# Optimization experiments

Measured on AMD Instinct MI355X. Metric: run time of the kernel, lower is better.

The kernel has to match this reference:

```python
import jax, jax.numpy as jnp
import numpy as np

B, S, D = 2, 2048, 1024   # batch, seq, hidden_dim
I = 512                   # intermediate_dim (per-expert FFN width)
E = 16                    # num_experts
TOP_K = 2


def setup_inputs() -> dict:
    key = jax.random.key(0)
    ks = jax.random.split(key, 10)
    sc_d = 1.0 / np.sqrt(D)
    sc_i = 1.0 / np.sqrt(I)
    return {
        "x": jax.random.normal(ks[0], (B, S, D), dtype=jnp.float32),
        # router gate: Linear(D -> E) with bias (nnx.Linear default)
        "gate_w": jax.random.normal(ks[1], (D, E), dtype=jnp.float32) * sc_d,
        "gate_b": jnp.zeros((E,), dtype=jnp.float32),
        # shared expert MLP (SwiGLU: down(silu(gate(x)) * up(x)))
        "shared_wg": jax.random.normal(ks[2], (D, I), dtype=jnp.float32) * sc_d,
        "shared_wu": jax.random.normal(ks[3], (D, I), dtype=jnp.float32) * sc_d,
        "shared_wd": jax.random.normal(ks[4], (I, D), dtype=jnp.float32) * sc_i,
        # routed experts, stacked on leading E axis
        "experts_wg": jax.random.normal(ks[5], (E, D, I), dtype=jnp.float32) * sc_d,
        "experts_wu": jax.random.normal(ks[6], (E, D, I), dtype=jnp.float32) * sc_d,
        "experts_wd": jax.random.normal(ks[7], (E, I, D), dtype=jnp.float32) * sc_i,
    }


def _mlp(x, wg, wu, wd):
    # SwiGLU MLP: down(silu(gate(x)) * up(x))
    return jnp.einsum("bsi,id->bsd", jax.nn.silu(x @ wg) * (x @ wu), wd)


def reference(x, gate_w, gate_b, shared_wg, shared_wu, shared_wd,
              experts_wg, experts_wu, experts_wd):
    # router: sigmoid logits -> top_k -> normalize by sum of selected scores
    router_logits = jax.nn.sigmoid(x @ gate_w + gate_b)          # [B,S,E]
    expert_values, expert_indices = jax.lax.top_k(router_logits, k=TOP_K)
    expert_values = expert_values / jnp.sum(expert_values, axis=-1, keepdims=True)

    # dense all-expert compute (faithful to source): [B,S,E,D]
    hg = jnp.einsum("bsd,edi->bsei", x, experts_wg)
    hu = jnp.einsum("bsd,edi->bsei", x, experts_wu)
    all_outputs = jnp.einsum("bsei,eid->bsed", jax.nn.silu(hg) * hu, experts_wd)

    # gather top-k expert outputs: [B,S,K,D]
    selected = jnp.take_along_axis(all_outputs, expert_indices[..., None], axis=2)
    expert_weighted = jnp.sum(expert_values[..., None] * selected, axis=2)  # [B,S,D]

    return x + _mlp(x, shared_wg, shared_wu, shared_wd) + expert_weighted
```

## Files before the change

kernel.cpp:

```cpp
#include <hip/hip_runtime.h>
#include <stdint.h>

typedef __attribute__((ext_vector_type(8))) short short8;
typedef __attribute__((ext_vector_type(4))) float f32x4;

#define TOKENS 4096
#define DDIM 1024
#define IDIM 512
#define NEXP 16
#define NEXP1 17
#define CSTRIDE 32
#define MAXMB 112

#define OFF_WGU   0ull
#define OFF_WD    35651584ull
#define OFF_XB    53477376ull
#define OFF_HGU   61865984ull
#define OFF_H     87031808ull
#define OFF_TOK   99614720ull
#define OFF_REC   99893248ull
#define OFF_WREC  99926016ull
#define OFF_CNT   100171776ull
#define OFF_BASE  100175872ull

__device__ __forceinline__ float bf2f(unsigned short u) {
    union { uint32_t i; float f; } v; v.i = ((uint32_t)u) << 16; return v.f;
}
__device__ __forceinline__ unsigned short f2bf(float f) {
    union { float f; uint32_t i; } v; v.f = f;
    uint32_t r = v.i + 0x7FFFu + ((v.i >> 16) & 1u);
    return (unsigned short)(r >> 16);
}
__device__ __forceinline__ void cp16(const unsigned short* g, unsigned short* l) {
    __builtin_amdgcn_global_load_lds(
        (const __attribute__((address_space(1))) uint32_t*)g,
        (__attribute__((address_space(3))) uint32_t*)l, 16, 0, 0);
}

__global__ __launch_bounds__(256)
void k_transpose(const float* __restrict__ eg, const float* __restrict__ eu,
                 const float* __restrict__ ed, const float* __restrict__ sg,
                 const float* __restrict__ su, const float* __restrict__ sd,
                 unsigned short* __restrict__ Wgu, unsigned short* __restrict__ Wd)
{
    int z = blockIdx.z;
    int e = z / 3, m = z % 3;
    int R = (m == 2) ? 512 : 1024;
    int C = (m == 2) ? 1024 : 512;
    int r0 = blockIdx.y * 64, c0 = blockIdx.x * 64;
    if (r0 >= R || c0 >= C) return;
    const float* src;
    if (m == 0)      src = (e < 16) ? eg + (size_t)e * 524288 : sg;
    else if (m == 1) src = (e < 16) ? eu + (size_t)e * 524288 : su;
    else             src = (e < 16) ? ed + (size_t)e * 524288 : sd;

    __shared__ float tl[64 * 65];
    const int tid = threadIdx.x;

    {
        const int lr = tid >> 4;
        const int lc = (tid & 15) * 4;
        #pragma unroll
        for (int ps = 0; ps < 4; ++ps) {
            int r = ps * 16 + lr;
            float4 v = *(const float4*)(src + (size_t)(r0 + r) * C + (c0 + lc));
            float* d = &tl[r * 65 + lc];
            d[0] = v.x; d[1] = v.y; d[2] = v.z; d[3] = v.w;
        }
    }
    __syncthreads();

    {
        const int w = tid >> 6, l = tid & 63;
        const int kb = (l & 7) * 8;
        #pragma unroll
        for (int p = 0; p < 2; ++p) {
            int nl = p * 32 + w * 8 + (l >> 3);
            unsigned short ov[8];
            #pragma unroll
            for (int j = 0; j < 8; ++j)
                ov[j] = f2bf(tl[(kb + j) * 65 + nl]);
            int n = c0 + nl;
            int k = r0 + kb;
            unsigned short* dst;
            if (m < 2) dst = Wgu + (size_t)e * 1048576 + (size_t)(2 * n + m) * 1024 + k;
            else       dst = Wd  + (size_t)e * 524288  + (size_t)n * 512 + k;
            *(uint4*)dst = *(uint4*)ov;
        }
    }
}

__global__ void k_xconv(const float* __restrict__ x, unsigned short* __restrict__ xb,
                        int* __restrict__ tok)
{
    int i = blockIdx.x * 256 + threadIdx.x;
    float4 v = ((const float4*)x)[i];
    ushort4 b;
    b.x = f2bf(v.x); b.y = f2bf(v.y); b.z = f2bf(v.z); b.w = f2bf(v.w);
    ((ushort4*)xb)[i] = b;
    if (i < TOKENS) tok[16 * 4096 + i] = i;
}

__global__ __launch_bounds__(512, 4)
void k_router(const float* __restrict__ x, const float* __restrict__ gw,
              const float* __restrict__ gb, int* __restrict__ tok,
              int2* __restrict__ rec, float2* __restrict__ wrec,
              int* __restrict__ counts)
{
    __shared__ float gws[1024 * 12];

    const int t = blockIdx.x * 8 + (threadIdx.x >> 6);
    const int lane = threadIdx.x & 63;
    const float* xr = x + (size_t)t * DDIM;

    float xv[16];
    #pragma unroll
    for (int kk = 0; kk < 16; ++kk) xv[kk] = xr[kk * 64 + lane];

    float v[16];

    for (int p = 0; p < 2; ++p) {
        __syncthreads();
        #pragma unroll
        for (int c = 0; c < 4; ++c) {
            int idx = threadIdx.x + c * 512;
            int k = idx >> 1;
            int h = (idx & 1) * 4;
            float4 g4 = *(const float4*)(gw + k * 16 + p * 8 + h);
            *(float4*)&gws[k * 12 + h] = g4;
        }
        __syncthreads();

        double a[8];
        #pragma unroll
        for (int j = 0; j < 8; ++j) a[j] = 0.0;

        #pragma unroll
        for (int kk = 0; kk < 16; ++kk) {
            int kl = kk * 64 + lane;
            float4 gA = *(const float4*)&gws[kl * 12];
            float4 gB = *(const float4*)&gws[kl * 12 + 4];
            double xd = (double)xv[kk];
            a[0] += xd * (double)gA.x; a[1] += xd * (double)gA.y;
            a[2] += xd * (double)gA.z; a[3] += xd * (double)gA.w;
            a[4] += xd * (double)gB.x; a[5] += xd * (double)gB.y;
            a[6] += xd * (double)gB.z; a[7] += xd * (double)gB.w;
        }

        #pragma unroll
        for (int off = 32; off > 0; off >>= 1) {
            #pragma unroll
            for (int j = 0; j < 8; ++j)
                a[j] += __shfl_xor(a[j], off, 64);
        }

        #pragma unroll
        for (int j = 0; j < 8; ++j)
            v[p * 8 + j] = 1.0f / (1.0f + expf(-(float)(a[j] + (double)gb[p * 8 + j])));
    }

    if (lane == 0) {
        int i0 = 0;
        #pragma unroll
        for (int e = 1; e < 16; ++e) if (v[e] > v[i0]) i0 = e;
        int i1 = (i0 == 0) ? 1 : 0;
        #pragma unroll
        for (int e = 0; e < 16; ++e) if (e != i0 && e != i1 && v[e] > v[i1]) i1 = e;
        float s = v[i0] + v[i1];
        float w0 = v[i0] / s, w1 = v[i1] / s;
        int p0 = atomicAdd(&counts[i0 * CSTRIDE], 1);
        tok[i0 * 4096 + p0] = t;
        int p1 = atomicAdd(&counts[i1 * CSTRIDE], 1);
        tok[i1 * 4096 + p1] = t;
        rec[t]  = make_int2(i0 * 4096 + p0, i1 * 4096 + p1);
        wrec[t] = make_float2(w0, w1);
    }
}

__global__ void k_prefix(int* counts, int* bases, int* mbp)
{
    if (threadIdx.x == 0 && blockIdx.x == 0) {
        counts[16 * CSTRIDE] = TOKENS;
        int a = 0, b = 0;
        for (int e = 0; e < NEXP1; ++e) {
            int c = counts[e * CSTRIDE];
            bases[e] = a; a += c;
            mbp[e] = b;  b += (c + 127) >> 7;
        }
        bases[17] = a;
        mbp[17] = b;
    }
}

template <int MODE>
__global__ __launch_bounds__(256, 3)
void k_gemm(const unsigned short* __restrict__ Amat, const unsigned short* __restrict__ Bmat,
            const int* __restrict__ tok, const int* __restrict__ counts,
            const int* __restrict__ bases, const int* __restrict__ mbp,
            unsigned short* __restrict__ Out)
{
    constexpr int K = (MODE == 0) ? 1024 : 512;
    const int my = blockIdx.y;
    if (my >= mbp[17]) return;
    int e = 0;
    while (my >= mbp[e + 1]) ++e;
    const int cnt = counts[e * CSTRIDE];
    const int m0 = (my - mbp[e]) * 128;
    const int n0 = blockIdx.x * 128;
    const int base = bases[e];

    __shared__ unsigned short As0[128 * 32];
    __shared__ unsigned short As1[128 * 32];
    __shared__ unsigned short Bs0[128 * 32];
    __shared__ unsigned short Bs1[128 * 32];

    const int tid  = threadIdx.x;
    const int wave = tid >> 6;
    const int lane = tid & 63;
    const int lrow = lane >> 2;
    const int lseg = lane & 3;

    unsigned short* a0d0 = &As0[wave * 1024];
    unsigned short* a0d1 = &As0[wave * 1024 + 512];
    unsigned short* a1d0 = &As1[wave * 1024];
    unsigned short* a1d1 = &As1[wave * 1024 + 512];
    unsigned short* b0d0 = &Bs0[wave * 1024];
    unsigned short* b0d1 = &Bs0[wave * 1024 + 512];
    unsigned short* b1d0 = &Bs1[wave * 1024];
    unsigned short* b1d1 = &Bs1[wave * 1024 + 512];

    int ar0 = m0 + wave * 32 + lrow;      if (ar0 > cnt - 1) ar0 = cnt - 1;
    int ar1 = m0 + wave * 32 + 16 + lrow; if (ar1 > cnt - 1) ar1 = cnt - 1;
    size_t ai0, ai1;
    if (MODE == 0) { ai0 = (size_t)tok[e * 4096 + ar0]; ai1 = (size_t)tok[e * 4096 + ar1]; }
    else           { ai0 = (size_t)(base + ar0);        ai1 = (size_t)(base + ar1); }
    const unsigned short* ag0 = Amat + ai0 * K + lseg * 8;
    const unsigned short* ag1 = Amat + ai1 * K + lseg * 8;
    const size_t eoff = (size_t)e * 1024 * K;
    const unsigned short* bg0 = Bmat + eoff + (size_t)(n0 + wave * 32 + lrow) * K + lseg * 8;
    const unsigned short* bg1 = Bmat + eoff + (size_t)(n0 + wave * 32 + 16 + lrow) * K + lseg * 8;

    const int wm = wave & 1, wn = wave >> 1;
    const int q = lane >> 4, mc = lane & 15;

    f32x4 acc[4][4];
    #pragma unroll
    for (int i = 0; i < 4; ++i)
        #pragma unroll
        for (int j = 0; j < 4; ++j) acc[i][j] = (f32x4){0.f, 0.f, 0.f, 0.f};

    for (int k0 = 0; k0 < K; k0 += 64) {
        __syncthreads();
        cp16(ag0 + k0,      a0d0);
        cp16(ag0 + k0 + 32, a1d0);
        cp16(ag1 + k0,      a0d1);
        cp16(ag1 + k0 + 32, a1d1);
        cp16(bg0 + k0,      b0d0);
        cp16(bg0 + k0 + 32, b1d0);
        cp16(bg1 + k0,      b0d1);
        cp16(bg1 + k0 + 32, b1d1);
        __syncthreads();
        short8 a0[4], b0[4], a1[4], b1[4];
        #pragma unroll
        for (int i = 0; i < 4; ++i) {
            a0[i] = *(const short8*)&As0[(wm * 64 + i * 16 + mc) * 32 + q * 8];
            a1[i] = *(const short8*)&As1[(wm * 64 + i * 16 + mc) * 32 + q * 8];
        }
        #pragma unroll
        for (int j = 0; j < 4; ++j) {
            b0[j] = *(const short8*)&Bs0[(wn * 64 + j * 16 + mc) * 32 + q * 8];
            b1[j] = *(const short8*)&Bs1[(wn * 64 + j * 16 + mc) * 32 + q * 8];
        }
        #pragma unroll
        for (int i = 0; i < 4; ++i)
            #pragma unroll
            for (int j = 0; j < 4; ++j)
                acc[i][j] = __builtin_amdgcn_mfma_f32_16x16x32_bf16(a0[i], b0[j], acc[i][j], 0, 0, 0);
        #pragma unroll
        for (int i = 0; i < 4; ++i)
            #pragma unroll
            for (int j = 0; j < 4; ++j)
                acc[i][j] = __builtin_amdgcn_mfma_f32_16x16x32_bf16(a1[i], b1[j], acc[i][j], 0, 0, 0);
    }

    #pragma unroll
    for (int i = 0; i < 4; ++i) {
        int lr = wm * 64 + i * 16 + q * 4;
        #pragma unroll
        for (int r = 0; r < 4; ++r) {
            int mrow = m0 + lr + r;
            if (mrow >= cnt) continue;
            #pragma unroll
            for (int j = 0; j < 4; ++j) {
                int gc = n0 + wn * 64 + j * 16 + mc;
                float val = acc[i][j][r];
                if (MODE == 0) {
                    float other = __shfl_xor(val, 1, 64);
                    float g = (mc & 1) ? other : val;
                    float u = (mc & 1) ? val : other;
                    float h = g / (1.0f + __expf(-g)) * u;
                    if ((mc & 1) == 0)
                        Out[(size_t)(base + mrow) * 512 + (gc >> 1)] = f2bf(h);
                } else {
                    Out[(size_t)(base + mrow) * 1024 + gc] = f2bf(val);
                }
            }
        }
    }
}

__global__ void k_combine(const float* __restrict__ x, const unsigned short* __restrict__ Hs,
                          const int2* __restrict__ rec, const float2* __restrict__ wrec,
                          const int* __restrict__ bases, float* __restrict__ out)
{
    int t = blockIdx.x * 2 + (threadIdx.x >> 7);
    int c = (threadIdx.x & 127) * 8;
    int2 r = rec[t];
    float2 w = wrec[t];
    int s0 = bases[r.x >> 12] + (r.x & 4095);
    int s1 = bases[r.y >> 12] + (r.y & 4095);
    int ss = 8192 + t;

    unsigned short h0[8], h1[8], hs[8];
    *(uint4*)h0 = *(const uint4*)(Hs + (size_t)s0 * 1024 + c);
    *(uint4*)h1 = *(const uint4*)(Hs + (size_t)s1 * 1024 + c);
    *(uint4*)hs = *(const uint4*)(Hs + (size_t)ss * 1024 + c);
    const float* xr = x + (size_t)t * 1024 + c;
    float o[8];
    #pragma unroll
    for (int j = 0; j < 8; ++j)
        o[j] = xr[j] + bf2f(hs[j]) + w.x * bf2f(h0[j]) + w.y * bf2f(h1[j]);
    float* orow = out + (size_t)t * 1024 + c;
    *(float4*)orow       = *(float4*)&o[0];
    *(float4*)(orow + 4) = *(float4*)&o[4];
}

extern "C" void kernel_launch(void* const* d_in, const int* in_sizes, int n_in,
                              void* d_out, int out_size, void* d_ws, size_t ws_size,
                              hipStream_t stream)
{
    const float* x  = (const float*)d_in[0];
    const float* gw = (const float*)d_in[1];
    const float* gb = (const float*)d_in[2];
    const float* sg = (const float*)d_in[3];
    const float* su = (const float*)d_in[4];
    const float* sd = (const float*)d_in[5];
    const float* eg = (const float*)d_in[6];
    const float* eu = (const float*)d_in[7];
    const float* ed = (const float*)d_in[8];
    float* out = (float*)d_out;
    char* ws = (char*)d_ws;

    unsigned short* Wgu = (unsigned short*)(ws + OFF_WGU);
    unsigned short* Wd  = (unsigned short*)(ws + OFF_WD);
    unsigned short* xb  = (unsigned short*)(ws + OFF_XB);
    unsigned short* Hgu = (unsigned short*)(ws + OFF_HGU);
    unsigned short* H   = (unsigned short*)(ws + OFF_H);
    int*    tok   = (int*)(ws + OFF_TOK);
    int2*   rec   = (int2*)(ws + OFF_REC);
    float2* wrec  = (float2*)(ws + OFF_WREC);
    int*    counts= (int*)(ws + OFF_CNT);
    int*    bases = (int*)(ws + OFF_BASE);
    int*    mbp   = bases + 20;

    hipMemsetAsync(counts, 0, 4096, stream);
    k_transpose<<<dim3(16, 16, 51), 256, 0, stream>>>(eg, eu, ed, sg, su, sd, Wgu, Wd);
    k_xconv<<<4096, 256, 0, stream>>>(x, xb, tok);
    k_router<<<512, 512, 0, stream>>>(x, gw, gb, tok, rec, wrec, counts);
    k_prefix<<<1, 64, 0, stream>>>(counts, bases, mbp);
    k_gemm<0><<<dim3(8, MAXMB), 256, 0, stream>>>(xb, Wgu, tok, counts, bases, mbp, H);
    k_gemm<1><<<dim3(8, MAXMB), 256, 0, stream>>>(H, Wd, tok, counts, bases, mbp, Hgu);
    k_combine<<<2048, 256, 0, stream>>>(x, Hgu, rec, wrec, bases, out);
}
```

Measured before the change: 282.6 us.

## Double-buffer LDS tiles with prefetch and XOR-swizzle shared memory layout

```diff
diff --git a/kernel.cpp b/kernel.cpp
--- a/kernel.cpp
+++ b/kernel.cpp
@@ -192,8 +192,45 @@
     }
 }
 
+
+#define STAGE8(BUF, KK) do {                                                  \
+    cp16(ag0 + (KK),      &As[BUF][0][wb]);                                   \
+    cp16(ag0 + (KK) + 32, &As[BUF][1][wb]);                                   \
+    cp16(ag1 + (KK),      &As[BUF][0][wb + 512]);                             \
+    cp16(ag1 + (KK) + 32, &As[BUF][1][wb + 512]);                             \
+    cp16(bg0 + (KK),      &Bs[BUF][0][wb]);                                   \
+    cp16(bg0 + (KK) + 32, &Bs[BUF][1][wb]);                                   \
+    cp16(bg1 + (KK),      &Bs[BUF][0][wb + 512]);                             \
+    cp16(bg1 + (KK) + 32, &Bs[BUF][1][wb + 512]);                             \
+} while (0)
+
+#define GSTEP(BUF, PRE, KNEXT) do {                                           \
+    if (PRE) STAGE8((BUF) ^ 1, KNEXT);                                        \
+    short8 va0[4], va1[4], vb0[4], vb1[4];                                    \
+    _Pragma("unroll")                                                         \
+    for (int i = 0; i < 4; ++i) {                                             \
+        va0[i] = *(const short8*)&As[BUF][0][(wm*64 + i*16 + mc)*32 + qs];    \
+        va1[i] = *(const short8*)&As[BUF][1][(wm*64 + i*16 + mc)*32 + qs];    \
+    }                                                                         \
+    _Pragma("unroll")                                                         \
+    for (int j = 0; j < 4; ++j) {                                             \
+        vb0[j] = *(const short8*)&Bs[BUF][0][(wn*64 + j*16 + mc)*32 + qs];    \
+        vb1[j] = *(const short8*)&Bs[BUF][1][(wn*64 + j*16 + mc)*32 + qs];    \
+    }                                                                         \
+    _Pragma("unroll")                                                         \
+    for (int i = 0; i < 4; ++i)                                               \
+        _Pragma("unroll")                                                     \
+        for (int j = 0; j < 4; ++j)                                           \
+            acc[i][j] = __builtin_amdgcn_mfma_f32_16x16x32_bf16(va0[i], vb0[j], acc[i][j], 0, 0, 0); \
+    _Pragma("unroll")                                                         \
+    for (int i = 0; i < 4; ++i)                                               \
+        _Pragma("unroll")                                                     \
+        for (int j = 0; j < 4; ++j)                                           \
+            acc[i][j] = __builtin_amdgcn_mfma_f32_16x16x32_bf16(va1[i], vb1[j], acc[i][j], 0, 0, 0); \
+} while (0)
+
 template <int MODE>
-__global__ __launch_bounds__(256, 3)
+__global__ __launch_bounds__(256, 2)
 void k_gemm(const unsigned short* __restrict__ Amat, const unsigned short* __restrict__ Bmat,
             const int* __restrict__ tok, const int* __restrict__ counts,
             const int* __restrict__ bases, const int* __restrict__ mbp,
@@ -209,25 +246,16 @@
     const int n0 = blockIdx.x * 128;
     const int base = bases[e];
 
-    __shared__ unsigned short As0[128 * 32];
-    __shared__ unsigned short As1[128 * 32];
-    __shared__ unsigned short Bs0[128 * 32];
-    __shared__ unsigned short Bs1[128 * 32];
+    __shared__ unsigned short As[2][2][128 * 32];
+    __shared__ unsigned short Bs[2][2][128 * 32];
 
     const int tid  = threadIdx.x;
     const int wave = tid >> 6;
     const int lane = tid & 63;
     const int lrow = lane >> 2;
-    const int lseg = lane & 3;
-
-    unsigned short* a0d0 = &As0[wave * 1024];
-    unsigned short* a0d1 = &As0[wave * 1024 + 512];
-    unsigned short* a1d0 = &As1[wave * 1024];
-    unsigned short* a1d1 = &As1[wave * 1024 + 512];
-    unsigned short* b0d0 = &Bs0[wave * 1024];
-    unsigned short* b0d1 = &Bs0[wave * 1024 + 512];
-    unsigned short* b1d0 = &Bs1[wave * 1024];
-    unsigned short* b1d1 = &Bs1[wave * 1024 + 512];
+    const int lseg = (lane & 3) ^ ((lrow >> 1) & 3);
+
+    const int wb = wave * 1024;
 
     int ar0 = m0 + wave * 32 + lrow;      if (ar0 > cnt - 1) ar0 = cnt - 1;
     int ar1 = m0 + wave * 32 + 16 + lrow; if (ar1 > cnt - 1) ar1 = cnt - 1;
@@ -242,6 +270,7 @@
 
     const int wm = wave & 1, wn = wave >> 1;
     const int q = lane >> 4, mc = lane & 15;
+    const int qs = (q ^ ((mc >> 1) & 3)) * 8;
 
     f32x4 acc[4][4];
     #pragma unroll
@@ -249,38 +278,14 @@
         #pragma unroll
         for (int j = 0; j < 4; ++j) acc[i][j] = (f32x4){0.f, 0.f, 0.f, 0.f};
 
-    for (int k0 = 0; k0 < K; k0 += 64) {
+    STAGE8(0, 0);
+    __syncthreads();
+
+    for (int k0 = 0; k0 < K; k0 += 128) {
+        GSTEP(0, 1, k0 + 64);
         __syncthreads();
-        cp16(ag0 + k0,      a0d0);
-        cp16(ag0 + k0 + 32, a1d0);
-        cp16(ag1 + k0,      a0d1);
-        cp16(ag1 + k0 + 32, a1d1);
-        cp16(bg0 + k0,      b0d0);
-        cp16(bg0 + k0 + 32, b1d0);
-        cp16(bg1 + k0,      b0d1);
-        cp16(bg1 + k0 + 32, b1d1);
+        GSTEP(1, (k0 + 128 < K), k0 + 128);
         __syncthreads();
-        short8 a0[4], b0[4], a1[4], b1[4];
-        #pragma unroll
-        for (int i = 0; i < 4; ++i) {
-            a0[i] = *(const short8*)&As0[(wm * 64 + i * 16 + mc) * 32 + q * 8];
-            a1[i] = *(const short8*)&As1[(wm * 64 + i * 16 + mc) * 32 + q * 8];
-        }
-        #pragma unroll
-        for (int j = 0; j < 4; ++j) {
-            b0[j] = *(const short8*)&Bs0[(wn * 64 + j * 16 + mc) * 32 + q * 8];
-            b1[j] = *(const short8*)&Bs1[(wn * 64 + j * 16 + mc) * 32 + q * 8];
-        }
-        #pragma unroll
-        for (int i = 0; i < 4; ++i)
-            #pragma unroll
-            for (int j = 0; j < 4; ++j)
-                acc[i][j] = __builtin_amdgcn_mfma_f32_16x16x32_bf16(a0[i], b0[j], acc[i][j], 0, 0, 0);
-        #pragma unroll
-        for (int i = 0; i < 4; ++i)
-            #pragma unroll
-            for (int j = 0; j < 4; ++j)
-                acc[i][j] = __builtin_amdgcn_mfma_f32_16x16x32_bf16(a1[i], b1[j], acc[i][j], 0, 0, 0);
     }
 
     #pragma unroll
```

After: 289.3 us. 1.02x slower.

## Fuse transpose, x conversion, router and prefix into one front kernel

Applied to the files above, without the earlier changes.

```diff
diff --git a/kernel.cpp b/kernel.cpp
--- a/kernel.cpp
+++ b/kernel.cpp
@@ -23,6 +23,8 @@
 #define OFF_CNT   100171776ull
 #define OFF_BASE  100175872ull
 
+#define TICKET_IDX 768
+
 __device__ __forceinline__ float bf2f(unsigned short u) {
     union { uint32_t i; float f; } v; v.i = ((uint32_t)u) << 16; return v.f;
 }
@@ -37,158 +39,170 @@
         (__attribute__((address_space(3))) uint32_t*)l, 16, 0, 0);
 }
 
-__global__ __launch_bounds__(256)
-void k_transpose(const float* __restrict__ eg, const float* __restrict__ eu,
-                 const float* __restrict__ ed, const float* __restrict__ sg,
-                 const float* __restrict__ su, const float* __restrict__ sd,
-                 unsigned short* __restrict__ Wgu, unsigned short* __restrict__ Wd)
+__global__ __launch_bounds__(512, 4)
+void k_front(const float* __restrict__ x, const float* __restrict__ gw,
+             const float* __restrict__ gb,
+             const float* __restrict__ eg, const float* __restrict__ eu,
+             const float* __restrict__ ed, const float* __restrict__ sg,
+             const float* __restrict__ su, const float* __restrict__ sd,
+             unsigned short* __restrict__ Wgu, unsigned short* __restrict__ Wd,
+             unsigned short* __restrict__ xb, int* __restrict__ tok,
+             int2* __restrict__ rec, float2* __restrict__ wrec,
+             int* __restrict__ counts, int* __restrict__ bases, int* __restrict__ mbp)
 {
-    int z = blockIdx.z;
-    int e = z / 3, m = z % 3;
-    int R = (m == 2) ? 512 : 1024;
-    int C = (m == 2) ? 1024 : 512;
-    int r0 = blockIdx.y * 64, c0 = blockIdx.x * 64;
-    if (r0 >= R || c0 >= C) return;
-    const float* src;
-    if (m == 0)      src = (e < 16) ? eg + (size_t)e * 524288 : sg;
-    else if (m == 1) src = (e < 16) ? eu + (size_t)e * 524288 : su;
-    else             src = (e < 16) ? ed + (size_t)e * 524288 : sd;
-
-    __shared__ float tl[64 * 65];
+    __shared__ union {
+        float gws[1024 * 12];
+        float tl[2][64 * 65];
+    } sm;
+
+    const int bid = blockIdx.x;
     const int tid = threadIdx.x;
 
-    {
-        const int lr = tid >> 4;
-        const int lc = (tid & 15) * 4;
-        #pragma unroll
-        for (int ps = 0; ps < 4; ++ps) {
-            int r = ps * 16 + lr;
-            float4 v = *(const float4*)(src + (size_t)(r0 + r) * C + (c0 + lc));
-            float* d = &tl[r * 65 + lc];
-            d[0] = v.x; d[1] = v.y; d[2] = v.z; d[3] = v.w;
+    if (bid < 512) {
+        {
+            const int b0 = bid * 2048;
+            #pragma unroll
+            for (int c = 0; c < 4; ++c) {
+                int i = b0 + c * 512 + tid;
+                float4 v = ((const float4*)x)[i];
+                ushort4 b;
+                b.x = f2bf(v.x); b.y = f2bf(v.y); b.z = f2bf(v.z); b.w = f2bf(v.w);
+                ((ushort4*)xb)[i] = b;
+            }
+            if (tid < 8) tok[16 * 4096 + bid * 8 + tid] = bid * 8 + tid;
+        }
+
+        const int t = bid * 8 + (tid >> 6);
+        const int lane = tid & 63;
+        const float* xr = x + (size_t)t * DDIM;
+
+        float xv[16];
+        #pragma unroll
+        for (int kk = 0; kk < 16; ++kk) xv[kk] = xr[kk * 64 + lane];
+
+        float v[16];
+
+        for (int p = 0; p < 2; ++p) {
+            __syncthreads();
+            #pragma unroll
+            for (int c = 0; c < 4; ++c) {
+                int idx = tid + c * 512;
+                int k = idx >> 1;
+                int h = (idx & 1) * 4;
+                float4 g4 = *(const float4*)(gw + k * 16 + p * 8 + h);
+                *(float4*)&sm.gws[k * 12 + h] = g4;
+            }
+            __syncthreads();
+
+            double a[8];
+            #pragma unroll
+            for (int j = 0; j < 8; ++j) a[j] = 0.0;
+
+            #pragma unroll
+            for (int kk = 0; kk < 16; ++kk) {
+                int kl = kk * 64 + lane;
+                float4 gA = *(const float4*)&sm.gws[kl * 12];
+                float4 gB = *(const float4*)&sm.gws[kl * 12 + 4];
+                double xd = (double)xv[kk];
+                a[0] += xd * (double)gA.x; a[1] += xd * (double)gA.y;
+                a[2] += xd * (double)gA.z; a[3] += xd * (double)gA.w;
+                a[4] += xd * (double)gB.x; a[5] += xd * (double)gB.y;
+                a[6] += xd * (double)gB.z; a[7] += xd * (double)gB.w;
+            }
+
+            #pragma unroll
+            for (int off = 32; off > 0; off >>= 1) {
+                #pragma unroll
+                for (int j = 0; j < 8; ++j)
+                    a[j] += __shfl_xor(a[j], off, 64);
+            }
+
+            #pragma unroll
+            for (int j = 0; j < 8; ++j)
+                v[p * 8 + j] = 1.0f / (1.0f + expf(-(float)(a[j] + (double)gb[p * 8 + j])));
+        }
+
+        if (lane == 0) {
+            int i0 = 0;
+            #pragma unroll
+            for (int e = 1; e < 16; ++e) if (v[e] > v[i0]) i0 = e;
+            int i1 = (i0 == 0) ? 1 : 0;
+            #pragma unroll
+            for (int e = 0; e < 16; ++e) if (e != i0 && e != i1 && v[e] > v[i1]) i1 = e;
+            float s = v[i0] + v[i1];
+            float w0 = v[i0] / s, w1 = v[i1] / s;
+            int p0 = atomicAdd(&counts[i0 * CSTRIDE], 1);
+            tok[i0 * 4096 + p0] = t;
+            int p1 = atomicAdd(&counts[i1 * CSTRIDE], 1);
+            tok[i1 * 4096 + p1] = t;
+            rec[t]  = make_int2(i0 * 4096 + p0, i1 * 4096 + p1);
+            wrec[t] = make_float2(w0, w1);
+        }
+    } else {
+        const int tau = (bid - 512) * 2 + (tid >> 8);
+        const int z = tau >> 7;
+        const int rem = tau & 127;
+        const int e = z / 3, m = z % 3;
+        int ty, tx;
+        if (m == 2) { ty = rem >> 4; tx = rem & 15; }
+        else        { ty = rem >> 3; tx = rem & 7;  }
+        const int C = (m == 2) ? 1024 : 512;
+        const int r0 = ty * 64, c0 = tx * 64;
+        const float* src;
+        if (m == 0)      src = (e < 16) ? eg + (size_t)e * 524288 : sg;
+        else if (m == 1) src = (e < 16) ? eu + (size_t)e * 524288 : su;
+        else             src = (e < 16) ? ed + (size_t)e * 524288 : sd;
+
+        float* tlp = sm.tl[tid >> 8];
+        const int tt = tid & 255;
+
+        {
+            const int lr = tt >> 4;
+            const int lc = (tt & 15) * 4;
+            #pragma unroll
+            for (int ps = 0; ps < 4; ++ps) {
+                int r = ps * 16 + lr;
+                float4 vv = *(const float4*)(src + (size_t)(r0 + r) * C + (c0 + lc));
+                float* d = &tlp[r * 65 + lc];
+                d[0] = vv.x; d[1] = vv.y; d[2] = vv.z; d[3] = vv.w;
+            }
+        }
+        __syncthreads();
+
+        {
+            const int w = tt >> 6, l = tt & 63;
+            const int kb = (l & 7) * 8;
+            #pragma unroll
+            for (int p = 0; p < 2; ++p) {
+                int nl = p * 32 + w * 8 + (l >> 3);
+                unsigned short ov[8];
+                #pragma unroll
+                for (int j = 0; j < 8; ++j)
+                    ov[j] = f2bf(tlp[(kb + j) * 65 + nl]);
+                int n = c0 + nl;
+                int k = r0 + kb;
+                unsigned short* dst;
+                if (m < 2) dst = Wgu + (size_t)e * 1048576 + (size_t)(2 * n + m) * 1024 + k;
+                else       dst = Wd  + (size_t)e * 524288  + (size_t)n * 512 + k;
+                *(uint4*)dst = *(uint4*)ov;
+            }
         }
     }
+
     __syncthreads();
-
-    {
-        const int w = tid >> 6, l = tid & 63;
-        const int kb = (l & 7) * 8;
-        #pragma unroll
-        for (int p = 0; p < 2; ++p) {
-            int nl = p * 32 + w * 8 + (l >> 3);
-            unsigned short ov[8];
-            #pragma unroll
-            for (int j = 0; j < 8; ++j)
-                ov[j] = f2bf(tl[(kb + j) * 65 + nl]);
-            int n = c0 + nl;
-            int k = r0 + kb;
-            unsigned short* dst;
-            if (m < 2) dst = Wgu + (size_t)e * 1048576 + (size_t)(2 * n + m) * 1024 + k;
-            else       dst = Wd  + (size_t)e * 524288  + (size_t)n * 512 + k;
-            *(uint4*)dst = *(uint4*)ov;
-        }
-    }
-}
-
-__global__ void k_xconv(const float* __restrict__ x, unsigned short* __restrict__ xb,
-                        int* __restrict__ tok)
-{
-    int i = blockIdx.x * 256 + threadIdx.x;
-    float4 v = ((const float4*)x)[i];
-    ushort4 b;
-    b.x = f2bf(v.x); b.y = f2bf(v.y); b.z = f2bf(v.z); b.w = f2bf(v.w);
-    ((ushort4*)xb)[i] = b;
-    if (i < TOKENS) tok[16 * 4096 + i] = i;
-}
-
-__global__ __launch_bounds__(512, 4)
-void k_router(const float* __restrict__ x, const float* __restrict__ gw,
-              const float* __restrict__ gb, int* __restrict__ tok,
-              int2* __restrict__ rec, float2* __restrict__ wrec,
-              int* __restrict__ counts)
-{
-    __shared__ float gws[1024 * 12];
-
-    const int t = blockIdx.x * 8 + (threadIdx.x >> 6);
-    const int lane = threadIdx.x & 63;
-    const float* xr = x + (size_t)t * DDIM;
-
-    float xv[16];
-    #pragma unroll
-    for (int kk = 0; kk < 16; ++kk) xv[kk] = xr[kk * 64 + lane];
-
-    float v[16];
-
-    for (int p = 0; p < 2; ++p) {
-        __syncthreads();
-        #pragma unroll
-        for (int c = 0; c < 4; ++c) {
-            int idx = threadIdx.x + c * 512;
-            int k = idx >> 1;
-            int h = (idx & 1) * 4;
-            float4 g4 = *(const float4*)(gw + k * 16 + p * 8 + h);
-            *(float4*)&gws[k * 12 + h] = g4;
-        }
-        __syncthreads();
-
-        double a[8];
-        #pragma unroll
-        for (int j = 0; j < 8; ++j) a[j] = 0.0;
-
-        #pragma unroll
-        for (int kk = 0; kk < 16; ++kk) {
-            int kl = kk * 64 + lane;
-            float4 gA = *(const float4*)&gws[kl * 12];
-            float4 gB = *(const float4*)&gws[kl * 12 + 4];
-            double xd = (double)xv[kk];
-            a[0] += xd * (double)gA.x; a[1] += xd * (double)gA.y;
-            a[2] += xd * (double)gA.z; a[3] += xd * (double)gA.w;
-            a[4] += xd * (double)gB.x; a[5] += xd * (double)gB.y;
-            a[6] += xd * (double)gB.z; a[7] += xd * (double)gB.w;
-        }
-
-        #pragma unroll
-        for (int off = 32; off > 0; off >>= 1) {
-            #pragma unroll
-            for (int j = 0; j < 8; ++j)
-                a[j] += __shfl_xor(a[j], off, 64);
-        }
-
-        #pragma unroll
-        for (int j = 0; j < 8; ++j)
-            v[p * 8 + j] = 1.0f / (1.0f + expf(-(float)(a[j] + (double)gb[p * 8 + j])));
-    }
-
-    if (lane == 0) {
-        int i0 = 0;
-        #pragma unroll
-        for (int e = 1; e < 16; ++e) if (v[e] > v[i0]) i0 = e;
-        int i1 = (i0 == 0) ? 1 : 0;
-        #pragma unroll
-        for (int e = 0; e < 16; ++e) if (e != i0 && e != i1 && v[e] > v[i1]) i1 = e;
-        float s = v[i0] + v[i1];
-        float w0 = v[i0] / s, w1 = v[i1] / s;
-        int p0 = atomicAdd(&counts[i0 * CSTRIDE], 1);
-        tok[i0 * 4096 + p0] = t;
-        int p1 = atomicAdd(&counts[i1 * CSTRIDE], 1);
-        tok[i1 * 4096 + p1] = t;
-        rec[t]  = make_int2(i0 * 4096 + p0, i1 * 4096 + p1);
-        wrec[t] = make_float2(w0, w1);
-    }
-}
-
-__global__ void k_prefix(int* counts, int* bases, int* mbp)
-{
-    if (threadIdx.x == 0 && blockIdx.x == 0) {
-        counts[16 * CSTRIDE] = TOKENS;
-        int a = 0, b = 0;
-        for (int e = 0; e < NEXP1; ++e) {
-            int c = counts[e * CSTRIDE];
-            bases[e] = a; a += c;
-            mbp[e] = b;  b += (c + 127) >> 7;
-        }
-        bases[17] = a;
-        mbp[17] = b;
+    if (tid == 0) {
+        __threadfence();
+        if (atomicAdd(&counts[TICKET_IDX], 1) == (int)gridDim.x - 1) {
+            counts[16 * CSTRIDE] = TOKENS;
+            int a = 0, b = 0;
+            for (int e = 0; e < NEXP1; ++e) {
+                int c = (e < 16) ? atomicAdd(&counts[e * CSTRIDE], 0) : TOKENS;
+                bases[e] = a; a += c;
+                mbp[e] = b;  b += (c + 127) >> 7;
+            }
+            bases[17] = a;
+            mbp[17] = b;
+        }
     }
 }
 
@@ -363,11 +377,9 @@
     int*    bases = (int*)(ws + OFF_BASE);
     int*    mbp   = bases + 20;
 
-    hipMemsetAsync(counts, 0, 4096, stream);
-    k_transpose<<<dim3(16, 16, 51), 256, 0, stream>>>(eg, eu, ed, sg, su, sd, Wgu, Wd);
-    k_xconv<<<4096, 256, 0, stream>>>(x, xb, tok);
-    k_router<<<512, 512, 0, stream>>>(x, gw, gb, tok, rec, wrec, counts);
-    k_prefix<<<1, 64, 0, stream>>>(counts, bases, mbp);
+    (void)hipMemsetAsync(counts, 0, 4096, stream);
+    k_front<<<3776, 512, 0, stream>>>(x, gw, gb, eg, eu, ed, sg, su, sd,
+                                      Wgu, Wd, xb, tok, rec, wrec, counts, bases, mbp);
     k_gemm<0><<<dim3(8, MAXMB), 256, 0, stream>>>(xb, Wgu, tok, counts, bases, mbp, H);
     k_gemm<1><<<dim3(8, MAXMB), 256, 0, stream>>>(H, Wd, tok, counts, bases, mbp, Hgu);
     k_combine<<<2048, 256, 0, stream>>>(x, Hgu, rec, wrec, bases, out);
```

Result: slower. 462.9 us (+63.8%).

## Fuse x conversion, router and prefix scan into one kernel with last-block ticket

Applied to the files above, without the earlier changes.

```diff
diff --git a/kernel.cpp b/kernel.cpp
--- a/kernel.cpp
+++ b/kernel.cpp
@@ -23,6 +23,8 @@
 #define OFF_CNT   100171776ull
 #define OFF_BASE  100175872ull
 
+#define TICKET_IDX 768
+
 __device__ __forceinline__ float bf2f(unsigned short u) {
     union { uint32_t i; float f; } v; v.i = ((uint32_t)u) << 16; return v.f;
 }
@@ -90,27 +92,33 @@
     }
 }
 
-__global__ void k_xconv(const float* __restrict__ x, unsigned short* __restrict__ xb,
-                        int* __restrict__ tok)
-{
-    int i = blockIdx.x * 256 + threadIdx.x;
-    float4 v = ((const float4*)x)[i];
-    ushort4 b;
-    b.x = f2bf(v.x); b.y = f2bf(v.y); b.z = f2bf(v.z); b.w = f2bf(v.w);
-    ((ushort4*)xb)[i] = b;
-    if (i < TOKENS) tok[16 * 4096 + i] = i;
-}
-
-__global__ __launch_bounds__(512, 4)
-void k_router(const float* __restrict__ x, const float* __restrict__ gw,
-              const float* __restrict__ gb, int* __restrict__ tok,
-              int2* __restrict__ rec, float2* __restrict__ wrec,
-              int* __restrict__ counts)
-{
-    __shared__ float gws[1024 * 12];
-
-    const int t = blockIdx.x * 8 + (threadIdx.x >> 6);
-    const int lane = threadIdx.x & 63;
+__global__ __launch_bounds__(512, 3)
+void k_route(const float* __restrict__ x, const float* __restrict__ gw,
+             const float* __restrict__ gb, unsigned short* __restrict__ xb,
+             int* __restrict__ tok, int2* __restrict__ rec,
+             float2* __restrict__ wrec, int* __restrict__ counts,
+             int* __restrict__ bases, int* __restrict__ mbp)
+{
+    __shared__ float gws[1024 * 13];
+
+    const int bid = blockIdx.x;
+    const int tid = threadIdx.x;
+
+    {
+        const int b0 = bid * 2048;
+        #pragma unroll
+        for (int c = 0; c < 4; ++c) {
+            int i = b0 + c * 512 + tid;
+            float4 v = ((const float4*)x)[i];
+            ushort4 b;
+            b.x = f2bf(v.x); b.y = f2bf(v.y); b.z = f2bf(v.z); b.w = f2bf(v.w);
+            ((ushort4*)xb)[i] = b;
+        }
+        if (tid < 8) tok[16 * 4096 + bid * 8 + tid] = bid * 8 + tid;
+    }
+
+    const int t = bid * 8 + (tid >> 6);
+    const int lane = tid & 63;
     const float* xr = x + (size_t)t * DDIM;
 
     float xv[16];
@@ -123,11 +131,11 @@
         __syncthreads();
         #pragma unroll
         for (int c = 0; c < 4; ++c) {
-            int idx = threadIdx.x + c * 512;
+            int idx = tid + c * 512;
             int k = idx >> 1;
             int h = (idx & 1) * 4;
             float4 g4 = *(const float4*)(gw + k * 16 + p * 8 + h);
-            *(float4*)&gws[k * 12 + h] = g4;
+            *(float4*)&gws[k * 13 + h] = g4;
         }
         __syncthreads();
 
@@ -138,8 +146,8 @@
         #pragma unroll
         for (int kk = 0; kk < 16; ++kk) {
             int kl = kk * 64 + lane;
-            float4 gA = *(const float4*)&gws[kl * 12];
-            float4 gB = *(const float4*)&gws[kl * 12 + 4];
+            float4 gA = *(const float4*)&gws[kl * 13];
+            float4 gB = *(const float4*)&gws[kl * 13 + 4];
             double xd = (double)xv[kk];
             a[0] += xd * (double)gA.x; a[1] += xd * (double)gA.y;
             a[2] += xd * (double)gA.z; a[3] += xd * (double)gA.w;
@@ -175,20 +183,21 @@
         rec[t]  = make_int2(i0 * 4096 + p0, i1 * 4096 + p1);
         wrec[t] = make_float2(w0, w1);
     }
-}
-
-__global__ void k_prefix(int* counts, int* bases, int* mbp)
-{
-    if (threadIdx.x == 0 && blockIdx.x == 0) {
-        counts[16 * CSTRIDE] = TOKENS;
-        int a = 0, b = 0;
-        for (int e = 0; e < NEXP1; ++e) {
-            int c = counts[e * CSTRIDE];
-            bases[e] = a; a += c;
-            mbp[e] = b;  b += (c + 127) >> 7;
-        }
-        bases[17] = a;
-        mbp[17] = b;
+
+    __syncthreads();
+    if (tid == 0) {
+        __threadfence();
+        if (atomicAdd(&counts[TICKET_IDX], 1) == (int)gridDim.x - 1) {
+            counts[16 * CSTRIDE] = TOKENS;
+            int a = 0, b = 0;
+            for (int e = 0; e < NEXP1; ++e) {
+                int c = (e < 16) ? atomicAdd(&counts[e * CSTRIDE], 0) : TOKENS;
+                bases[e] = a; a += c;
+                mbp[e] = b;  b += (c + 127) >> 7;
+            }
+            bases[17] = a;
+            mbp[17] = b;
+        }
     }
 }
 
@@ -363,11 +372,9 @@
     int*    bases = (int*)(ws + OFF_BASE);
     int*    mbp   = bases + 20;
 
-    hipMemsetAsync(counts, 0, 4096, stream);
+    (void)hipMemsetAsync(counts, 0, 4096, stream);
     k_transpose<<<dim3(16, 16, 51), 256, 0, stream>>>(eg, eu, ed, sg, su, sd, Wgu, Wd);
-    k_xconv<<<4096, 256, 0, stream>>>(x, xb, tok);
-    k_router<<<512, 512, 0, stream>>>(x, gw, gb, tok, rec, wrec, counts);
-    k_prefix<<<1, 64, 0, stream>>>(counts, bases, mbp);
+    k_route<<<512, 512, 0, stream>>>(x, gw, gb, xb, tok, rec, wrec, counts, bases, mbp);
     k_gemm<0><<<dim3(8, MAXMB), 256, 0, stream>>>(xb, Wgu, tok, counts, bases, mbp, H);
     k_gemm<1><<<dim3(8, MAXMB), 256, 0, stream>>>(H, Wd, tok, counts, bases, mbp, Hgu);
     k_combine<<<2048, 256, 0, stream>>>(x, Hgu, rec, wrec, bases, out);
```

Measured after the change: 291.3 us. 3.1% more time.
